# Kernel optimization log

Hardware: AMD Instinct MI355X
Metric: run time of the kernel (lower is better)

## Reference

```python
import jax, jax.numpy as jnp
import numpy as np

K, STRIDE, PAD = 3, 1, 1
THRESH = 0.5  # STE binarization threshold on optical intensity


def _unfold(x, k, stride, pad):
    # x: (B, C, H, W) -> patches (B, L, C*k*k), torch.F.unfold channel ordering (C, kh, kw)
    B, C, H, W = x.shape
    Ho = (H + 2 * pad - k) // stride + 1
    Wo = (W + 2 * pad - k) // stride + 1
    xp = jnp.pad(x, ((0, 0), (0, 0), (pad, pad), (pad, pad)))
    # stack the k*k shifted views; small fixed k loop, fully vectorized over B,C,H,W
    views = [xp[:, :, i:i + Ho * stride:stride, j:j + Wo * stride:stride]
             for i in range(k) for j in range(k)]
    p = jnp.stack(views, axis=2)                 # (B, C, k*k, Ho, Wo)
    p = p.reshape(B, C * k * k, Ho * Wo)         # (B, d, L)
    return p.transpose(0, 2, 1), Ho, Wo          # (B, L, d)


def setup_inputs() -> dict:
    key = jax.random.key(0)
    k1, k2, k3 = jax.random.split(key, 3)
    B, Cin, H, W_ = 32, 64, 56, 56
    Cout = 128
    d = Cin * K * K  # 576
    x = jax.random.normal(k1, (B, Cin, H, W_), dtype=jnp.float32)
    W = jax.random.normal(k2, (Cout, d), dtype=jnp.float32) * (1.0 / np.sqrt(d))
    b = jax.random.normal(k3, (Cout,), dtype=jnp.float32) * 0.1
    return {"x": x, "W": W, "b": b}


def reference(x, W, b):
    # 1) unfold (im2col): (B, L, d)
    patches, Ho, Wo = _unfold(x, K, STRIDE, PAD)
    B = x.shape[0]
    Cout = W.shape[0]
    # 2) all out_channels optical logic units fused into one contraction
    z = jnp.einsum('bld,od->bol', patches, W) + b[None, :, None]  # (B, O, L)
    intensity = jnp.sin(z) ** 2                                    # optical interference intensity in [0,1]
    # 3) straight-through estimator: forward = hard binary, backward = d(intensity)
    binary = (intensity > THRESH).astype(intensity.dtype)
    out = intensity + jax.lax.stop_gradient(binary - intensity)
    # 4) reshape back to feature map
    return out.reshape(B, Cout, Ho, Wo)
```

## Files before the change

kernel.cpp:

```cpp
#include <hip/hip_runtime.h>
#include <math.h>

#define B_    32
#define CIN   64
#define HH    56
#define WW    56
#define COUT  128
#define DD    576
#define KC    384
#define LPX   (HH*WW)
#define TOTAL (B_*COUT*LPX)
#define NX    (B_*CIN*LPX)
#define PW    58
#define PPL   (PW*PW)
#define NXP   (B_*CIN*PPL)
#define MARGIN 4e-4f

typedef __attribute__((ext_vector_type(8)))  short  short8;
typedef __attribute__((ext_vector_type(16))) float  float16v;

__device__ __forceinline__ unsigned short bf16_rne(float f) {
    unsigned u = __float_as_uint(f);
    unsigned r = u + 0x7FFFu + ((u >> 16) & 1u);
    return (unsigned short)(r >> 16);
}
__device__ __forceinline__ float bf16_to_f(unsigned short h) {
    return __uint_as_float(((unsigned)h) << 16);
}

__device__ __forceinline__ float np_sinf(float x) {
#pragma clang fp contract(off)
    const float rint_cvt = 0x1.8p+23f;
    float q = __fmul_rn(x, 0x1.45f306p-1f);
    q = __fadd_rn(q, rint_cvt);
    q = __fsub_rn(q, rint_cvt);
    float r = fmaf(q, -0x1.921fb0p+0f, x);
    r = fmaf(q, -0x1.5110b4p-22f, r);
    r = fmaf(q, -0x1.846988p-48f, r);
    float r2 = __fmul_rn(r, r);
    float s = fmaf(0x1.7d3bbcp-19f, r2, -0x1.a06bbap-13f);
    s = fmaf(s, r2, 0x1.11119ap-7f);
    s = fmaf(s, r2, -0x1.555556p-3f);
    s = __fmul_rn(s, r2);
    s = fmaf(s, r, r);
    float c = fmaf(0x1.98e616p-16f, r2, -0x1.6c06dcp-10f);
    c = fmaf(c, r2, 0x1.55553cp-5f);
    c = fmaf(c, r2, -0.5f);
    c = fmaf(c, r2, 1.0f);
    int iq = (int)q;
    float res = (iq & 1) ? c : s;
    unsigned sgn = ((unsigned)(iq & 2)) << 30;
    return __uint_as_float(__float_as_uint(res) ^ sgn);
}
__device__ __forceinline__ int dec_np(float z) {
    float s = np_sinf(z);
    return (__fmul_rn(s, s) > 0.5f) ? 1 : 0;
}

__global__ __launch_bounds__(256)
void prep_all(const float* __restrict__ x, const float* __restrict__ W,
              unsigned* __restrict__ xpad,
              unsigned short* __restrict__ Wph, unsigned short* __restrict__ Wpl) {
    int i4 = (blockIdx.x * 256 + threadIdx.x) * 4;
    if (i4 < COUT * DD) {
#pragma unroll
        for (int e = 0; e < 4; ++e) {
            int i = i4 + e;
            int o = i / DD, k = i - o * DD;
            float w = W[i];
            unsigned short h = bf16_rne(w);
            unsigned short l = bf16_rne(w - bf16_to_f(h));
            int k18 = k >> 5, kr = k & 31;
            int s = (kr >> 4) & 1, half = (kr >> 3) & 1, j = kr & 7;
            int lane = half * 32 + (o & 31);
            int ot = o >> 5;
            unsigned dst = ((((unsigned)(k18 * 4 + ot)) * 2 + s) * 64 + lane) * 8 + j;
            Wph[dst] = h;
            Wpl[dst] = l;
        }
    }
    if (i4 < NXP) {
        unsigned vv[4];
#pragma unroll
        for (int e = 0; e < 4; ++e) {
            int i = i4 + e;
            int bc = i / PPL;
            int r  = i - bc * PPL;
            int yy = r / PW;
            int xx = r - yy * PW;
            unsigned v = 0u;
            if (yy >= 1 && yy <= HH && xx >= 1 && xx <= WW) {
                float f = x[(size_t)bc * LPX + (yy - 1) * WW + (xx - 1)];
                unsigned short h = bf16_rne(f);
                unsigned short l = bf16_rne(f - bf16_to_f(h));
                v = (unsigned)h | ((unsigned)l << 16);
            }
            vv[e] = v;
        }
        *(uint4*)(xpad + i4) = *(uint4*)vv;
    }
}

#define FRAG(t, s, hf, ln)  (((t) * 1024) + ((s) * 512) + ((hf) * 256) + ((ln) * 8))
#define SMEM_FIX  18432
#define SMEM_LIST 16384
__global__ __launch_bounds__(256, 4)
void conv_mfma(const unsigned* __restrict__ xpad,
               const unsigned short* __restrict__ Wph,
               const unsigned short* __restrict__ Wpl,
               const float* __restrict__ bias,
               float* __restrict__ out,
               const float* __restrict__ x,
               const float* __restrict__ Wt) {
    __shared__ __align__(16) char smem[SMEM_FIX + SMEM_LIST + 16];
    unsigned short* sP    = (unsigned short*)smem;
    float*          sxB   = (float*)smem;
    float*          swB   = sxB + 4 * DD;
    unsigned short* llist = (unsigned short*)(smem + SMEM_FIX);
    unsigned*       lcnt  = (unsigned*)(smem + SMEM_FIX + SMEM_LIST);

    const int tid = threadIdx.x;
    if (tid == 0) *lcnt = 0;
    const int bid = (blockIdx.x & 7) * 196 + (blockIdx.x >> 3);
    const int pt0 = bid * 64;

    const int plane = tid & 15;
    const int pair  = tid >> 4;
    const int s_st  = pair >> 3;
    const int h_st  = (pair >> 2) & 1;
    const int j2_st = pair & 3;

    unsigned pbase[4];
#pragma unroll
    for (int r = 0; r < 4; ++r) {
        int gp = pt0 + plane + r * 16;
        int br = gp / LPX;
        int pr = gp - br * LPX;
        int ypx = pr / WW;
        int xpx = pr - ypx * WW;
        pbase[r] = (unsigned)(br * (CIN * PPL) + ypx * PW + xpx);
    }

    const int w    = tid >> 6;
    const int lane = tid & 63;
    const int lm   = lane & 31;
    const int half = lane >> 5;
    const uint4* wAh = (const uint4*)Wph + w * 128 + lane;
    const uint4* wAl = (const uint4*)Wpl + w * 128 + lane;

    float16v acc[2];
#pragma unroll
    for (int n = 0; n < 2; ++n)
#pragma unroll
        for (int i = 0; i < 16; ++i) acc[n][i] = 0.f;

    unsigned pg[4][2], pgn[4][2];
    uint4 Ah[2], Al[2], Ahn[2], Aln[2];

#define LOADP(K0, DST)                                                         \
    {                                                                          \
        int d0 = (K0) + pair * 2;                                              \
        int c0 = d0 / 9, t0 = d0 - c0 * 9;                                     \
        int u0 = t0 / 3, v0 = t0 - u0 * 3;                                     \
        int t1 = t0 + 1, c1 = c0;                                              \
        if (t1 == 9) { t1 = 0; c1 = c0 + 1; }                                  \
        int u1 = t1 / 3, v1 = t1 - u1 * 3;                                     \
        unsigned off0 = (unsigned)(c0 * PPL + u0 * PW + v0);                   \
        unsigned off1 = (unsigned)(c1 * PPL + u1 * PW + v1);                   \
        _Pragma("unroll")                                                      \
        for (int r = 0; r < 4; ++r) {                                          \
            DST[r][0] = xpad[pbase[r] + off0];                                 \
            DST[r][1] = xpad[pbase[r] + off1];                                 \
        }                                                                      \
    }

#define LOADA(IT, DH, DL)                                                      \
    _Pragma("unroll")                                                          \
    for (int s = 0; s < 2; ++s) {                                              \
        DH[s] = wAh[(IT) * 512 + s * 64];                                      \
        DL[s] = wAl[(IT) * 512 + s * 64];                                      \
    }

    LOADP(0, pg)
    LOADA(0, Ah, Al)

#pragma unroll
    for (int it = 0; it < 18; ++it) {
        unsigned short* bPh = sP + (it & 1) * 2048;
        unsigned short* bPl = sP + 4096 + (it & 1) * 2048;

#pragma unroll
        for (int r = 0; r < 4; ++r) {
            unsigned g0 = pg[r][0], g1 = pg[r][1];
            unsigned hw = (g0 & 0xFFFFu) | (g1 << 16);
            unsigned lw = (g0 >> 16) | (g1 & 0xFFFF0000u);
            int pm = plane + (r & 1) * 16;
            int word = (r >> 1) * 512 + s_st * 256 + h_st * 128 + pm * 4 + j2_st;
            ((unsigned*)bPh)[word] = hw;
            ((unsigned*)bPl)[word] = lw;
        }

        if (it < 17) {
            LOADA(it + 1, Ahn, Aln)
            LOADP((it + 1) * 32, pgn)
        }

        asm volatile("s_waitcnt lgkmcnt(0)" ::: "memory");
        __builtin_amdgcn_s_barrier();
        asm volatile("" ::: "memory");

#pragma unroll
        for (int n = 0; n < 2; ++n) {
            short8 Bh0 = *(const short8*)(bPh + FRAG(n, 0, half, lm));
            short8 Bl0 = *(const short8*)(bPl + FRAG(n, 0, half, lm));
            short8 Bh1 = *(const short8*)(bPh + FRAG(n, 1, half, lm));
            short8 Bl1 = *(const short8*)(bPl + FRAG(n, 1, half, lm));
            acc[n] = __builtin_amdgcn_mfma_f32_32x32x16_bf16(
                *(const short8*)&Ah[0], Bh0, acc[n], 0, 0, 0);
            acc[n] = __builtin_amdgcn_mfma_f32_32x32x16_bf16(
                *(const short8*)&Ah[0], Bl0, acc[n], 0, 0, 0);
            acc[n] = __builtin_amdgcn_mfma_f32_32x32x16_bf16(
                *(const short8*)&Al[0], Bh0, acc[n], 0, 0, 0);
            acc[n] = __builtin_amdgcn_mfma_f32_32x32x16_bf16(
                *(const short8*)&Ah[1], Bh1, acc[n], 0, 0, 0);
            acc[n] = __builtin_amdgcn_mfma_f32_32x32x16_bf16(
                *(const short8*)&Ah[1], Bl1, acc[n], 0, 0, 0);
            acc[n] = __builtin_amdgcn_mfma_f32_32x32x16_bf16(
                *(const short8*)&Al[1], Bh1, acc[n], 0, 0, 0);
        }

        if (it < 17) {
#pragma unroll
            for (int r = 0; r < 4; ++r) {
                pg[r][0] = pgn[r][0];
                pg[r][1] = pgn[r][1];
            }
#pragma unroll
            for (int s = 0; s < 2; ++s) {
                Ah[s] = Ahn[s];
                Al[s] = Aln[s];
            }
        }
    }
#undef LOADP
#undef LOADA

#pragma unroll
    for (int n = 0; n < 2; ++n) {
        const int gp0 = pt0 + n * 32;
        const int bpos = gp0 / LPX;
        const int pxb = gp0 - bpos * LPX + lm;
        const size_t outb = (size_t)bpos * COUT * LPX;
#pragma unroll
        for (int reg = 0; reg < 16; ++reg) {
            int o = w * 32 + 4 * half + (reg & 3) + 8 * (reg >> 2);
            float z = acc[n][reg] + bias[o];
            float q = rintf(__fmul_rn(z, 0.63661975f));
            float rr = fmaf(q, -1.5707964f, z);
            float d = fabsf(fabsf(rr) - 0.78539816f);
            size_t oidx = outb + (size_t)o * LPX + pxb;
            out[oidx] = (float)(((int)q) & 1);
            if (d < MARGIN) {
                unsigned p = atomicAdd(lcnt, 1u);
                llist[p] = (unsigned short)(tid * 32 + n * 16 + reg);
            }
        }
    }

    __syncthreads();
    const unsigned cnt = *lcnt;
    const int wv = w;
    for (unsigned base = 0; base < cnt; base += 4) {
        __syncthreads();
        unsigned ei = base + wv;
        int b_e = 0, o_e = 0, py_e = 0, px_e = 0;
        size_t idx_e = 0;
        if (ei < cnt) {
            unsigned e = llist[ei];
            int tid_e = e >> 5;
            int n_e   = (e >> 4) & 1;
            int reg_e = e & 15;
            o_e = ((tid_e >> 6) << 5) + 4 * ((tid_e & 63) >> 5)
                  + (reg_e & 3) + 8 * (reg_e >> 2);
            int gp = pt0 + n_e * 32 + (tid_e & 31);
            b_e = gp / LPX;
            int pix = gp - b_e * LPX;
            py_e = pix / WW;
            px_e = pix - py_e * WW;
            idx_e = (size_t)b_e * COUT * LPX + (size_t)o_e * LPX + pix;
            const float* xc = x  + ((size_t)(b_e * CIN + lane)) * LPX;
            const float* wc = Wt + (size_t)o_e * DD + lane * 9;
#pragma unroll
            for (int u = 0; u < 3; ++u)
#pragma unroll
                for (int v = 0; v < 3; ++v) {
                    int tp = u * 3 + v;
                    int gy = py_e + u - 1, gx = px_e + v - 1;
                    float p = ((unsigned)gy < HH && (unsigned)gx < WW)
                                  ? xc[gy * WW + gx] : 0.f;
                    sxB[wv * DD + lane * 9 + tp] = p;
                    swB[wv * DD + lane * 9 + tp] = wc[tp];
                }
        }
        __syncthreads();
        if (ei < cnt && lane == 0) {
            const float* px_ = sxB + wv * DD;
            const float* pw_ = swB + wv * DD;
            float accA = 0.f, accB2 = 0.f;
            for (int d = 0; d < KC; ++d)        accA  = fmaf(px_[d], pw_[d], accA);
            for (int d = KC; d < DD; ++d)       accB2 = fmaf(px_[d], pw_[d], accB2);
            float zG = __fadd_rn(accA, accB2);
            float z  = __fadd_rn(zG, bias[o_e]);
            out[idx_e] = (float)dec_np(z);
        }
    }
}

__global__ __launch_bounds__(256)
void np_emul_conv(const float* __restrict__ x,
                  const float* __restrict__ Wt,
                  const float* __restrict__ bias,
                  float* __restrict__ out) {
#pragma clang fp contract(off)
    int idx = blockIdx.x * 256 + threadIdx.x;
    if (idx >= TOTAL) return;
    int px = idx % WW;
    int t  = idx / WW;
    int py = t % HH;  t /= HH;
    int o  = t % COUT;
    int b  = t / COUT;
    const float* wrow = Wt + (size_t)o * DD;
    const float* xb   = x + (size_t)b * CIN * LPX;
    float accA = 0.f, accB2 = 0.f;
    for (int c = 0; c < CIN; ++c) {
        const float* xc = xb + c * LPX;
        const float* wc = wrow + c * 9;
        int dbase = c * 9;
#pragma unroll
        for (int u = 0; u < 3; ++u)
#pragma unroll
            for (int v = 0; v < 3; ++v) {
                int tp = u * 3 + v;
                int gy = py + u - 1, gx = px + v - 1;
                float p = ((unsigned)gy < HH && (unsigned)gx < WW) ? xc[gy * WW + gx] : 0.f;
                if (dbase + tp < KC) accA  = fmaf(p, wc[tp], accA);
                else                 accB2 = fmaf(p, wc[tp], accB2);
            }
    }
    float z = __fadd_rn(__fadd_rn(accA, accB2), bias[o]);
    out[idx] = (float)dec_np(z);
}

extern "C" void kernel_launch(void* const* d_in, const int* in_sizes, int n_in,
                              void* d_out, int out_size, void* d_ws, size_t ws_size,
                              hipStream_t stream) {
    const float* x  = (const float*)d_in[0];
    const float* Wt = (const float*)d_in[1];
    const float* bb = (const float*)d_in[2];
    float* out = (float*)d_out;

    const size_t WSPLIT = (size_t)COUT * DD * 2;
    const size_t XP     = (size_t)NXP * 4;
    const size_t FIXED  = 2 * WSPLIT + XP;

    if (ws_size >= FIXED + 4096) {
        unsigned short* Wph = (unsigned short*)d_ws;
        unsigned short* Wpl = Wph + COUT * DD;
        unsigned* xpad = (unsigned*)((char*)d_ws + 2 * WSPLIT);

        prep_all<<<dim3(NXP / 4 / 256), dim3(256), 0, stream>>>(x, Wt, xpad, Wph, Wpl);
        conv_mfma<<<dim3(1568), dim3(256), 0, stream>>>(xpad, Wph, Wpl, bb, out, x, Wt);
    } else {
        np_emul_conv<<<(TOTAL + 255) / 256, 256, 0, stream>>>(x, Wt, bb, out);
    }
}
```

Baseline: 169.1 us.

## Fuse bf16 hi/lo split and padding into the MFMA conv kernel

Removes the separate prep kernel that wrote a zero-padded, bf16-split copy of x and a pre-swizzled split of W to workspace. The conv kernel now reads raw fp32 x with bounds checks and raw fp32 W rows, and does the bf16 hi/lo rounding in registers before staging to LDS or feeding the MFMA. This saves one launch and a full write and read of the padded input buffer. In exchange it adds per-iteration ALU work for the split, branchy boundary loads, and uncoalesced float4 weight loads. The fallback path for small workspace is dropped.

```diff
diff --git a/kernel.cpp b/kernel.cpp
--- a/kernel.cpp
+++ b/kernel.cpp
@@ -10,23 +10,12 @@
 #define KC    384
 #define LPX   (HH*WW)
 #define TOTAL (B_*COUT*LPX)
-#define NX    (B_*CIN*LPX)
-#define PW    58
-#define PPL   (PW*PW)
-#define NXP   (B_*CIN*PPL)
 #define MARGIN 4e-4f
 
 typedef __attribute__((ext_vector_type(8)))  short  short8;
 typedef __attribute__((ext_vector_type(16))) float  float16v;
 
-__device__ __forceinline__ unsigned short bf16_rne(float f) {
-    unsigned u = __float_as_uint(f);
-    unsigned r = u + 0x7FFFu + ((u >> 16) & 1u);
-    return (unsigned short)(r >> 16);
-}
-__device__ __forceinline__ float bf16_to_f(unsigned short h) {
-    return __uint_as_float(((unsigned)h) << 16);
-}
+#define BRNE(u) ((u) + 0x7FFFu + (((u) >> 16) & 1u))
 
 __device__ __forceinline__ float np_sinf(float x) {
 #pragma clang fp contract(off)
@@ -57,61 +46,14 @@
     return (__fmul_rn(s, s) > 0.5f) ? 1 : 0;
 }
 
-__global__ __launch_bounds__(256)
-void prep_all(const float* __restrict__ x, const float* __restrict__ W,
-              unsigned* __restrict__ xpad,
-              unsigned short* __restrict__ Wph, unsigned short* __restrict__ Wpl) {
-    int i4 = (blockIdx.x * 256 + threadIdx.x) * 4;
-    if (i4 < COUT * DD) {
-#pragma unroll
-        for (int e = 0; e < 4; ++e) {
-            int i = i4 + e;
-            int o = i / DD, k = i - o * DD;
-            float w = W[i];
-            unsigned short h = bf16_rne(w);
-            unsigned short l = bf16_rne(w - bf16_to_f(h));
-            int k18 = k >> 5, kr = k & 31;
-            int s = (kr >> 4) & 1, half = (kr >> 3) & 1, j = kr & 7;
-            int lane = half * 32 + (o & 31);
-            int ot = o >> 5;
-            unsigned dst = ((((unsigned)(k18 * 4 + ot)) * 2 + s) * 64 + lane) * 8 + j;
-            Wph[dst] = h;
-            Wpl[dst] = l;
-        }
-    }
-    if (i4 < NXP) {
-        unsigned vv[4];
-#pragma unroll
-        for (int e = 0; e < 4; ++e) {
-            int i = i4 + e;
-            int bc = i / PPL;
-            int r  = i - bc * PPL;
-            int yy = r / PW;
-            int xx = r - yy * PW;
-            unsigned v = 0u;
-            if (yy >= 1 && yy <= HH && xx >= 1 && xx <= WW) {
-                float f = x[(size_t)bc * LPX + (yy - 1) * WW + (xx - 1)];
-                unsigned short h = bf16_rne(f);
-                unsigned short l = bf16_rne(f - bf16_to_f(h));
-                v = (unsigned)h | ((unsigned)l << 16);
-            }
-            vv[e] = v;
-        }
-        *(uint4*)(xpad + i4) = *(uint4*)vv;
-    }
-}
-
 #define FRAG(t, s, hf, ln)  (((t) * 1024) + ((s) * 512) + ((hf) * 256) + ((ln) * 8))
 #define SMEM_FIX  18432
 #define SMEM_LIST 16384
 __global__ __launch_bounds__(256, 4)
-void conv_mfma(const unsigned* __restrict__ xpad,
-               const unsigned short* __restrict__ Wph,
-               const unsigned short* __restrict__ Wpl,
-               const float* __restrict__ bias,
-               float* __restrict__ out,
-               const float* __restrict__ x,
-               const float* __restrict__ Wt) {
+void conv_fused(const float* __restrict__ x,
+                const float* __restrict__ Wt,
+                const float* __restrict__ bias,
+                float* __restrict__ out) {
     __shared__ __align__(16) char smem[SMEM_FIX + SMEM_LIST + 16];
     unsigned short* sP    = (unsigned short*)smem;
     float*          sxB   = (float*)smem;
@@ -130,23 +72,27 @@
     const int h_st  = (pair >> 2) & 1;
     const int j2_st = pair & 3;
 
+    const int bpos = pt0 / LPX;
+    const unsigned* xb = (const unsigned*)(x + (size_t)bpos * CIN * LPX);
+
+    int ypxA[4], xpxA[4];
     unsigned pbase[4];
 #pragma unroll
     for (int r = 0; r < 4; ++r) {
         int gp = pt0 + plane + r * 16;
-        int br = gp / LPX;
-        int pr = gp - br * LPX;
+        int pr = gp - bpos * LPX;
         int ypx = pr / WW;
         int xpx = pr - ypx * WW;
-        pbase[r] = (unsigned)(br * (CIN * PPL) + ypx * PW + xpx);
+        ypxA[r] = ypx;
+        xpxA[r] = xpx;
+        pbase[r] = (unsigned)(ypx * WW + xpx);
     }
 
     const int w    = tid >> 6;
     const int lane = tid & 63;
     const int lm   = lane & 31;
     const int half = lane >> 5;
-    const uint4* wAh = (const uint4*)Wph + w * 128 + lane;
-    const uint4* wAl = (const uint4*)Wpl + w * 128 + lane;
+    const float* wrow = Wt + (size_t)(w * 32 + lm) * DD + half * 8;
 
     float16v acc[2];
 #pragma unroll
@@ -155,7 +101,7 @@
         for (int i = 0; i < 16; ++i) acc[n][i] = 0.f;
 
     unsigned pg[4][2], pgn[4][2];
-    uint4 Ah[2], Al[2], Ahn[2], Aln[2];
+    float4 wA[4], wAn[4];
 
 #define LOADP(K0, DST)                                                         \
     {                                                                          \
@@ -165,24 +111,57 @@
         int t1 = t0 + 1, c1 = c0;                                              \
         if (t1 == 9) { t1 = 0; c1 = c0 + 1; }                                  \
         int u1 = t1 / 3, v1 = t1 - u1 * 3;                                     \
-        unsigned off0 = (unsigned)(c0 * PPL + u0 * PW + v0);                   \
-        unsigned off1 = (unsigned)(c1 * PPL + u1 * PW + v1);                   \
+        int off0 = c0 * LPX + (u0 - 1) * WW + (v0 - 1);                        \
+        int off1 = c1 * LPX + (u1 - 1) * WW + (v1 - 1);                        \
         _Pragma("unroll")                                                      \
         for (int r = 0; r < 4; ++r) {                                          \
-            DST[r][0] = xpad[pbase[r] + off0];                                 \
-            DST[r][1] = xpad[pbase[r] + off1];                                 \
+            int gy0 = ypxA[r] + u0 - 1, gx0 = xpxA[r] + v0 - 1;                \
+            int gy1 = ypxA[r] + u1 - 1, gx1 = xpxA[r] + v1 - 1;                \
+            DST[r][0] = ((unsigned)gy0 < HH && (unsigned)gx0 < WW)             \
+                            ? xb[pbase[r] + off0] : 0u;                        \
+            DST[r][1] = ((unsigned)gy1 < HH && (unsigned)gx1 < WW)             \
+                            ? xb[pbase[r] + off1] : 0u;                        \
         }                                                                      \
     }
 
-#define LOADA(IT, DH, DL)                                                      \
+#define LOADA(IT, DST)                                                         \
     _Pragma("unroll")                                                          \
     for (int s = 0; s < 2; ++s) {                                              \
-        DH[s] = wAh[(IT) * 512 + s * 64];                                      \
-        DL[s] = wAl[(IT) * 512 + s * 64];                                      \
+        DST[2 * s]     = *(const float4*)(wrow + (IT) * 32 + s * 16);          \
+        DST[2 * s + 1] = *(const float4*)(wrow + (IT) * 32 + s * 16 + 4);      \
+    }
+
+#define SPLITA(SRC, AH, AL)                                                    \
+    _Pragma("unroll")                                                          \
+    for (int s = 0; s < 2; ++s) {                                              \
+        unsigned fr0 = __float_as_uint(SRC[2 * s].x);                          \
+        unsigned fr1 = __float_as_uint(SRC[2 * s].y);                          \
+        unsigned fr2 = __float_as_uint(SRC[2 * s].z);                          \
+        unsigned fr3 = __float_as_uint(SRC[2 * s].w);                          \
+        unsigned fr4 = __float_as_uint(SRC[2 * s + 1].x);                      \
+        unsigned fr5 = __float_as_uint(SRC[2 * s + 1].y);                      \
+        unsigned fr6 = __float_as_uint(SRC[2 * s + 1].z);                      \
+        unsigned fr7 = __float_as_uint(SRC[2 * s + 1].w);                      \
+        unsigned fa[8] = {fr0, fr1, fr2, fr3, fr4, fr5, fr6, fr7};             \
+        _Pragma("unroll")                                                      \
+        for (int m = 0; m < 4; ++m) {                                          \
+            unsigned ua = fa[2 * m], ub = fa[2 * m + 1];                       \
+            unsigned r0a = BRNE(ua), r0b = BRNE(ub);                           \
+            ((unsigned*)&AH[s])[m] =                                           \
+                __builtin_amdgcn_perm(r0b, r0a, 0x07060302u);                  \
+            float lfa = __uint_as_float(ua) -                                  \
+                        __uint_as_float(r0a & 0xFFFF0000u);                    \
+            float lfb = __uint_as_float(ub) -                                  \
+                        __uint_as_float(r0b & 0xFFFF0000u);                    \
+            unsigned r1a = BRNE(__float_as_uint(lfa));                         \
+            unsigned r1b = BRNE(__float_as_uint(lfb));                         \
+            ((unsigned*)&AL[s])[m] =                                           \
+                __builtin_amdgcn_perm(r1b, r1a, 0x07060302u);                  \
+        }                                                                      \
     }
 
     LOADP(0, pg)
-    LOADA(0, Ah, Al)
+    LOADA(0, wA)
 
 #pragma unroll
     for (int it = 0; it < 18; ++it) {
@@ -191,9 +170,14 @@
 
 #pragma unroll
         for (int r = 0; r < 4; ++r) {
-            unsigned g0 = pg[r][0], g1 = pg[r][1];
-            unsigned hw = (g0 & 0xFFFFu) | (g1 << 16);
-            unsigned lw = (g0 >> 16) | (g1 & 0xFFFF0000u);
+            unsigned ua = pg[r][0], ub = pg[r][1];
+            unsigned r0a = BRNE(ua), r0b = BRNE(ub);
+            float lfa = __uint_as_float(ua) - __uint_as_float(r0a & 0xFFFF0000u);
+            float lfb = __uint_as_float(ub) - __uint_as_float(r0b & 0xFFFF0000u);
+            unsigned r1a = BRNE(__float_as_uint(lfa));
+            unsigned r1b = BRNE(__float_as_uint(lfb));
+            unsigned hw = __builtin_amdgcn_perm(r0b, r0a, 0x07060302u);
+            unsigned lw = __builtin_amdgcn_perm(r1b, r1a, 0x07060302u);
             int pm = plane + (r & 1) * 16;
             int word = (r >> 1) * 512 + s_st * 256 + h_st * 128 + pm * 4 + j2_st;
             ((unsigned*)bPh)[word] = hw;
@@ -201,13 +185,16 @@
         }
 
         if (it < 17) {
-            LOADA(it + 1, Ahn, Aln)
+            LOADA(it + 1, wAn)
             LOADP((it + 1) * 32, pgn)
         }
 
         asm volatile("s_waitcnt lgkmcnt(0)" ::: "memory");
         __builtin_amdgcn_s_barrier();
         asm volatile("" ::: "memory");
+
+        uint4 Ah[2], Al[2];
+        SPLITA(wA, Ah, Al)
 
 #pragma unroll
         for (int n = 0; n < 2; ++n) {
@@ -236,19 +223,16 @@
                 pg[r][1] = pgn[r][1];
             }
 #pragma unroll
-            for (int s = 0; s < 2; ++s) {
-                Ah[s] = Ahn[s];
-                Al[s] = Aln[s];
-            }
+            for (int s = 0; s < 4; ++s) wA[s] = wAn[s];
         }
     }
 #undef LOADP
 #undef LOADA
+#undef SPLITA
 
 #pragma unroll
     for (int n = 0; n < 2; ++n) {
         const int gp0 = pt0 + n * 32;
-        const int bpos = gp0 / LPX;
         const int pxb = gp0 - bpos * LPX + lm;
         const size_t outb = (size_t)bpos * COUT * LPX;
 #pragma unroll
@@ -273,7 +257,7 @@
     for (unsigned base = 0; base < cnt; base += 4) {
         __syncthreads();
         unsigned ei = base + wv;
-        int b_e = 0, o_e = 0, py_e = 0, px_e = 0;
+        int o_e = 0;
         size_t idx_e = 0;
         if (ei < cnt) {
             unsigned e = llist[ei];
@@ -283,10 +267,10 @@
             o_e = ((tid_e >> 6) << 5) + 4 * ((tid_e & 63) >> 5)
                   + (reg_e & 3) + 8 * (reg_e >> 2);
             int gp = pt0 + n_e * 32 + (tid_e & 31);
-            b_e = gp / LPX;
+            int b_e = gp / LPX;
             int pix = gp - b_e * LPX;
-            py_e = pix / WW;
-            px_e = pix - py_e * WW;
+            int py_e = pix / WW;
+            int px_e = pix - py_e * WW;
             idx_e = (size_t)b_e * COUT * LPX + (size_t)o_e * LPX + pix;
             const float* xc = x  + ((size_t)(b_e * CIN + lane)) * LPX;
             const float* wc = Wt + (size_t)o_e * DD + lane * 9;
@@ -304,6 +288,7 @@
         }
         __syncthreads();
         if (ei < cnt && lane == 0) {
+#pragma clang fp contract(off)
             const float* px_ = sxB + wv * DD;
             const float* pw_ = swB + wv * DD;
             float accA = 0.f, accB2 = 0.f;
@@ -316,41 +301,6 @@
     }
 }
 
-__global__ __launch_bounds__(256)
-void np_emul_conv(const float* __restrict__ x,
-                  const float* __restrict__ Wt,
-                  const float* __restrict__ bias,
-                  float* __restrict__ out) {
-#pragma clang fp contract(off)
-    int idx = blockIdx.x * 256 + threadIdx.x;
-    if (idx >= TOTAL) return;
-    int px = idx % WW;
-    int t  = idx / WW;
-    int py = t % HH;  t /= HH;
-    int o  = t % COUT;
-    int b  = t / COUT;
-    const float* wrow = Wt + (size_t)o * DD;
-    const float* xb   = x + (size_t)b * CIN * LPX;
-    float accA = 0.f, accB2 = 0.f;
-    for (int c = 0; c < CIN; ++c) {
-        const float* xc = xb + c * LPX;
-        const float* wc = wrow + c * 9;
-        int dbase = c * 9;
-#pragma unroll
-        for (int u = 0; u < 3; ++u)
-#pragma unroll
-            for (int v = 0; v < 3; ++v) {
-                int tp = u * 3 + v;
-                int gy = py + u - 1, gx = px + v - 1;
-                float p = ((unsigned)gy < HH && (unsigned)gx < WW) ? xc[gy * WW + gx] : 0.f;
-                if (dbase + tp < KC) accA  = fmaf(p, wc[tp], accA);
-                else                 accB2 = fmaf(p, wc[tp], accB2);
-            }
-    }
-    float z = __fadd_rn(__fadd_rn(accA, accB2), bias[o]);
-    out[idx] = (float)dec_np(z);
-}
-
 extern "C" void kernel_launch(void* const* d_in, const int* in_sizes, int n_in,
                               void* d_out, int out_size, void* d_ws, size_t ws_size,
                               hipStream_t stream) {
@@ -359,18 +309,5 @@
     const float* bb = (const float*)d_in[2];
     float* out = (float*)d_out;
 
-    const size_t WSPLIT = (size_t)COUT * DD * 2;
-    const size_t XP     = (size_t)NXP * 4;
-    const size_t FIXED  = 2 * WSPLIT + XP;
-
-    if (ws_size >= FIXED + 4096) {
-        unsigned short* Wph = (unsigned short*)d_ws;
-        unsigned short* Wpl = Wph + COUT * DD;
-        unsigned* xpad = (unsigned*)((char*)d_ws + 2 * WSPLIT);
-
-        prep_all<<<dim3(NXP / 4 / 256), dim3(256), 0, stream>>>(x, Wt, xpad, Wph, Wpl);
-        conv_mfma<<<dim3(1568), dim3(256), 0, stream>>>(xpad, Wph, Wpl, bb, out, x, Wt);
-    } else {
-        np_emul_conv<<<(TOTAL + 255) / 256, 256, 0, stream>>>(x, Wt, bb, out);
-    }
+    conv_fused<<<dim3(1568), dim3(256), 0, stream>>>(x, Wt, bb, out);
 }
```

Result: slower. 191.9 us (+13.5%).
